# Optimization experiments

Measured on AMD Instinct MI355X. Metric: run time of the kernel, lower is better.

## Reference

```python
import jax, jax.numpy as jnp
import numpy as np

# dims
P = 512          # perception_vector_size
A_DIM = 64       # action_vector_size
D_MODEL = 256
D_STATE = 16
D_CONV = 4
D_INNER = 2 * D_MODEL      # expand=2 -> 512
DT_RANK = D_MODEL // 16    # ceil(256/16) = 16
BATCH = 8192


def setup_inputs() -> dict:
    key = jax.random.key(0)
    ks = jax.random.split(key, 12)
    s = lambda k, shp, sc=0.02: (jax.random.normal(k, shp, jnp.float32) * sc)
    return {
        "perception": jax.random.normal(ks[0], (BATCH, P), jnp.float32),
        # Brain linears
        "W_in": s(ks[1], (D_MODEL, P)), "b_in": jnp.zeros((D_MODEL,), jnp.float32),
        "mu_w": s(ks[2], (A_DIM, D_MODEL)), "mu_b": jnp.zeros((A_DIM,), jnp.float32),
        "ls_w": s(ks[3], (A_DIM, D_MODEL)), "ls_b": jnp.zeros((A_DIM,), jnp.float32),
        # Mamba params (mamba_ssm Mamba(d_model=256, d_state=16, d_conv=4, expand=2))
        "in_proj_w": s(ks[4], (2 * D_INNER, D_MODEL)),            # no bias
        "conv_w": s(ks[5], (D_INNER, D_CONV), 0.1),               # depthwise causal conv
        "conv_b": jnp.zeros((D_INNER,), jnp.float32),
        "x_proj_w": s(ks[6], (DT_RANK + 2 * D_STATE, D_INNER)),   # no bias
        "dt_proj_w": s(ks[7], (D_INNER, DT_RANK), 0.1),
        "dt_proj_b": s(ks[8], (D_INNER,), 0.1),
        # S4D real init: A_log[d, n] = log(n+1)
        "A_log": jnp.log(jnp.broadcast_to(jnp.arange(1, D_STATE + 1, dtype=jnp.float32), (D_INNER, D_STATE))),
        "Dskip": jnp.ones((D_INNER,), jnp.float32),
        "out_proj_w": s(ks[9], (D_MODEL, D_INNER)),               # no bias
    }


def _mamba(x, in_proj_w, conv_w, conv_b, x_proj_w, dt_proj_w, dt_proj_b, A_log, Dskip):
    # x: [B, L, d_model]
    Bsz, L, _ = x.shape
    xz = x @ in_proj_w.T                       # [B, L, 2*D_INNER]
    u, z = jnp.split(xz, 2, axis=-1)           # each [B, L, D_INNER]
    # causal depthwise conv1d (padding d_conv-1 on the left), then SiLU
    u_pad = jnp.pad(u, ((0, 0), (D_CONV - 1, 0), (0, 0)))
    idx = jnp.arange(L)[:, None] + jnp.arange(D_CONV)[None, :]   # [L, K]
    windows = u_pad[:, idx, :]                 # [B, L, K, D_INNER]
    u = jnp.einsum('blkc,ck->blc', windows, conv_w) + conv_b
    u = jax.nn.silu(u)
    # input-dependent SSM params
    x_dbl = u @ x_proj_w.T                     # [B, L, dt_rank + 2*d_state]
    dt, Bm, Cm = jnp.split(x_dbl, [DT_RANK, DT_RANK + D_STATE], axis=-1)
    delta = jax.nn.softplus(dt @ dt_proj_w.T + dt_proj_b)  # [B, L, D_INNER]
    A = -jnp.exp(A_log)                        # [D_INNER, D_STATE]

    def step(h, inp):
        u_t, dl, b_t, c_t = inp                # [B,D],[B,D],[B,N],[B,N]
        dA = jnp.exp(dl[..., None] * A)        # [B, D, N]
        h = dA * h + dl[..., None] * b_t[:, None, :] * u_t[..., None]
        y = jnp.einsum('bdn,bn->bd', h, c_t)
        return h, y

    h0 = jnp.zeros((Bsz, D_INNER, D_STATE), u.dtype)
    xs = (u.transpose(1, 0, 2), delta.transpose(1, 0, 2),
          Bm.transpose(1, 0, 2), Cm.transpose(1, 0, 2))
    _, ys = jax.lax.scan(step, h0, xs)         # ys: [L, B, D_INNER]
    y = ys.transpose(1, 0, 2) + Dskip * u      # skip connection D*u
    return y * jax.nn.silu(z)


def reference(perception, W_in, b_in, mu_w, mu_b, ls_w, ls_b,
              in_proj_w, conv_w, conv_b, x_proj_w, dt_proj_w, dt_proj_b,
              A_log, Dskip, out_proj_w):
    x = (perception @ W_in.T + b_in)[:, None, :]     # [B, 1, d_model]
    y = _mamba(x, in_proj_w, conv_w, conv_b, x_proj_w,
               dt_proj_w, dt_proj_b, A_log, Dskip)   # [B, 1, D_INNER]
    h = (y @ out_proj_w.T)[:, 0, :]                  # [B, d_model]
    mu = jnp.tanh(h @ mu_w.T + mu_b)
    log_std = jnp.clip(h @ ls_w.T + ls_b, -5.0, 2.0)
    return mu, log_std
```

## Files before the change

### kernel.cpp

```cpp
#include <hip/hip_runtime.h>
#include <hip/hip_fp16.h>
#include <cmath>

#define BATCH 8192

typedef short bf16x8 __attribute__((ext_vector_type(8)));
typedef float f32x4 __attribute__((ext_vector_type(4)));
typedef float f32x16 __attribute__((ext_vector_type(16)));

__device__ __forceinline__ void split2(float x, unsigned short& h, unsigned short& l){
    unsigned u = __float_as_uint(x);
    unsigned hr = u + 0x7fffu + ((u >> 16) & 1u);
    unsigned short hs = (unsigned short)(hr >> 16);
    float hf = __uint_as_float(((unsigned)hs) << 16);
    float d = x - hf;
    unsigned v = __float_as_uint(d);
    unsigned short ls = (unsigned short)((v + 0x7fffu + ((v >> 16) & 1u)) >> 16);
    h = hs; l = ls;
}
__device__ __forceinline__ float fsig(float x){ return 1.f / (1.f + __expf(-x)); }
__device__ __forceinline__ float ftanh(float x){
    x = fminf(fmaxf(x, -10.f), 10.f);
    const float e = __expf(2.f*x);
    return (e - 1.f) / (e + 1.f);
}


__global__ __launch_bounds__(256) void prep_all(
    const float* __restrict__ percep,
    const float* __restrict__ in_proj, const float* __restrict__ W_in,
    const float* __restrict__ b_in,
    const float* __restrict__ mu_w, const float* __restrict__ ls_w,
    const float* __restrict__ conv_w, const float* __restrict__ conv_b,
    const float* __restrict__ out_proj, const float* __restrict__ x_proj,
    unsigned short* __restrict__ W1h, unsigned short* __restrict__ W1l,
    unsigned short* __restrict__ Wth, unsigned short* __restrict__ Wtl,
    unsigned short* __restrict__ Xph, unsigned short* __restrict__ Xpl,
    unsigned short* __restrict__ Ph, unsigned short* __restrict__ Pl,
    float* __restrict__ b1)
{
    __shared__ float As[16][33];
    __shared__ float Ws[16][36];
    __shared__ unsigned short Lh[4096];
    __shared__ unsigned short Ll[4096];

    const int bx = blockIdx.x, by = blockIdx.y;
    const int tid = threadIdx.x;

    if (bx >= 38){
        const int s = (bx-38)*16 + by;
        const int band = s >> 4, ks = s & 15;
        const size_t tbase = (size_t)s*4096;
#pragma unroll
        for (int g=0; g<2; ++g){
            const int u = g*256 + tid;
            const int row = u >> 2, piece = u & 3;
            const float* src = percep + (size_t)(band*128 + row)*512 + ks*32 + piece*8;
            const float4 v0 = *reinterpret_cast<const float4*>(src);
            const float4 v1 = *reinterpret_cast<const float4*>(src+4);
            unsigned short h[8], l[8];
            split2(v0.x,h[0],l[0]); split2(v0.y,h[1],l[1]);
            split2(v0.z,h[2],l[2]); split2(v0.w,h[3],l[3]);
            split2(v1.x,h[4],l[4]); split2(v1.y,h[5],l[5]);
            split2(v1.z,h[6],l[6]); split2(v1.w,h[7],l[7]);
            uint4 H, L;
            H.x=(unsigned)h[0]|((unsigned)h[1]<<16); H.y=(unsigned)h[2]|((unsigned)h[3]<<16);
            H.z=(unsigned)h[4]|((unsigned)h[5]<<16); H.w=(unsigned)h[6]|((unsigned)h[7]<<16);
            L.x=(unsigned)l[0]|((unsigned)l[1]<<16); L.y=(unsigned)l[2]|((unsigned)l[3]<<16);
            L.z=(unsigned)l[4]|((unsigned)l[5]<<16); L.w=(unsigned)l[6]|((unsigned)l[7]<<16);
            const int off = piece*1024 + row*8;
            *reinterpret_cast<uint4*>(&Lh[off]) = H;
            *reinterpret_cast<uint4*>(&Ll[off]) = L;
        }
        __syncthreads();
#pragma unroll
        for (int g=0; g<2; ++g){
            const int f = g*256 + tid;
            *reinterpret_cast<uint4*>(&Ph[tbase + f*8]) = *reinterpret_cast<const uint4*>(&Lh[f*8]);
            *reinterpret_cast<uint4*>(&Pl[tbase + f*8]) = *reinterpret_cast<const uint4*>(&Ll[f*8]);
        }
        return;
    }
    if (bx == 36){
        const int lane = tid & 63, w = tid >> 6;
        const float4 bv = *reinterpret_cast<const float4*>(&b_in[lane*4]);
        const int nbase = by*64 + w*16;
#pragma unroll 4
        for (int i=0;i<16;i++){
            const int n = nbase + i;
            const float4 av = *reinterpret_cast<const float4*>(&in_proj[(size_t)n*256 + lane*4]);
            float p = av.x*bv.x + av.y*bv.y + av.z*bv.z + av.w*bv.w;
#pragma unroll
            for (int off=32; off; off>>=1) p += __shfl_xor(p, off, 64);
            if (lane == 0)
                b1[n] = (n < 512) ? fmaf(p, conv_w[n*4+3], conv_b[n]) : p;
        }
        return;
    }
    if (bx == 37){
        const int c0 = by*32;
#pragma unroll
        for (int p=0;p<8;p++){
            const int idx = p*256 + tid;
            const int rrow = idx >> 5;
            const int c = c0 + (idx & 31);
            const float v = (rrow < 48) ? x_proj[(size_t)rrow*512 + c] : 0.f;
            unsigned short h,l; split2(v,h,l);
            const int ks = c >> 5, r = (c >> 3) & 3, pos = c & 7;
            const size_t off = (size_t)ks*2048 + (r*64 + rrow)*8 + pos;
            Xph[off]=h; Xpl[off]=l;
        }
        return;
    }
    const float* A; unsigned short *Oh, *Ol; int m0; bool wt;
    const float* B;
    if (bx < 32){ A = in_proj + (size_t)bx*32*256; B = W_in; Oh=W1h; Ol=W1l; m0=bx*32; wt=false; }
    else {
        const int t = bx - 32;
        A = (t < 2) ? (mu_w + (size_t)t*32*256) : (ls_w + (size_t)(t-2)*32*256);
        B = out_proj; Oh=Wth; Ol=Wtl; m0=t*32; wt=true;
    }
    const int n0 = by*32;

    const int tm = tid >> 3, tn = tid & 7;
    float acc[4] = {0.f,0.f,0.f,0.f};

    for (int k0=0;k0<256;k0+=16){
        {
            const int row = tid >> 3, kf = (tid & 7)*2;
            const float2 v = *reinterpret_cast<const float2*>(A + (size_t)row*256 + k0 + kf);
            As[kf][row] = v.x; As[kf+1][row] = v.y;
        }
        {
            const int kk = tid >> 4, c = (tid & 15)*2;
            const float2 v = *reinterpret_cast<const float2*>(B + (size_t)(k0+kk)*512 + n0 + c);
            Ws[kk][c] = v.x; Ws[kk][c+1] = v.y;
        }
        __syncthreads();
#pragma unroll
        for (int k=0;k<16;k++){
            const float a = As[k][tm];
            const float4 bv = *reinterpret_cast<const float4*>(&Ws[k][tn*4]);
            acc[0] = fmaf(a, bv.x, acc[0]);
            acc[1] = fmaf(a, bv.y, acc[1]);
            acc[2] = fmaf(a, bv.z, acc[2]);
            acc[3] = fmaf(a, bv.w, acc[3]);
        }
        __syncthreads();
    }
    {
        const int gm = m0 + tm;
        const float s = (!wt && gm < 512) ? conv_w[gm*4+3] : 1.f;
        const int n = n0 + tn*4;
        unsigned short h[4], l[4];
#pragma unroll
        for (int j=0;j<4;j++) split2(acc[j]*s, h[j], l[j]);
        const int ks = n >> 5, r = (n >> 3) & 3, pos = n & 7;
        size_t off;
        if (wt) off = (size_t)ks*4096 + (r*128 + gm)*8 + pos;
        else    off = (size_t)((gm>>7)*16 + ks)*4096 + (r*128 + (gm&127))*8 + pos;
        *reinterpret_cast<ushort4*>(&Oh[off]) = make_ushort4(h[0],h[1],h[2],h[3]);
        *reinterpret_cast<ushort4*>(&Ol[off]) = make_ushort4(l[0],l[1],l[2],l[3]);
    }
}

__global__ __launch_bounds__(256,8) void mgemm6c(
    const unsigned short* __restrict__ AhT, const unsigned short* __restrict__ AlT,
    const unsigned short* __restrict__ BhT, const unsigned short* __restrict__ BlT,
    const float* __restrict__ bias,
    float* __restrict__ O0, __half* __restrict__ O1)
{
    constexpr int NK = 16;

    const int tid = threadIdx.x;
    const int mb = blockIdx.x, nb = blockIdx.y;
    const int m0 = mb * 32, n0 = nb * 128;
    const int lane = tid & 63, wid = tid >> 6;
    const int half = lane >> 5, l32 = lane & 31;
    const int wn = wid * 32;

    f32x16 acc;
#pragma unroll
    for (int r=0;r<16;r++) acc[r] = 0.f;

    const int gm = m0 + l32;
    const size_t Atile0 = (size_t)((gm>>7)*16)*4096;
    const int Ain = (gm & 127)*8;
    const unsigned short* Bh0 = BhT + (size_t)nb*NK*4096;
    const unsigned short* Bl0 = BlT + (size_t)nb*NK*4096;

#pragma unroll
    for (int k=0; k<NK; ++k){
        const size_t at = Atile0 + (size_t)k*4096 + Ain;
        bf16x8 ah[2], al[2], bh[2], bl[2];
#pragma unroll
        for (int j=0;j<2;j++){
            const int r = j*2 + half;
            ah[j] = *reinterpret_cast<const bf16x8*>(&AhT[at + r*1024]);
            al[j] = *reinterpret_cast<const bf16x8*>(&AlT[at + r*1024]);
            const size_t off = (size_t)k*4096 + (r*128 + wn + l32)*8;
            bh[j] = *reinterpret_cast<const bf16x8*>(&Bh0[off]);
            bl[j] = *reinterpret_cast<const bf16x8*>(&Bl0[off]);
        }
#pragma unroll
        for (int j=0;j<2;j++){
            acc = __builtin_amdgcn_mfma_f32_32x32x16_bf16(ah[j], bh[j], acc, 0,0,0);
            acc = __builtin_amdgcn_mfma_f32_32x32x16_bf16(al[j], bh[j], acc, 0,0,0);
            acc = __builtin_amdgcn_mfma_f32_32x32x16_bf16(ah[j], bl[j], acc, 0,0,0);
        }
    }

#pragma unroll
    for (int r=0; r<16; ++r){
        const int row = m0 + (r&3) + 8*(r>>2) + 4*half;
        const int col = n0 + wn + l32;
        float v = acc[r] + bias[col];
        if (col < 512) O0[(size_t)row*512 + col] = v * fsig(v);
        else           O1[(size_t)row*512 + (col-512)] = __float2half(v);
    }
}

__global__ __launch_bounds__(256,2) void tail_fused3(
    const float* __restrict__ Uf, const __half* __restrict__ Zh,
    const unsigned short* __restrict__ XphT, const unsigned short* __restrict__ XplT,
    const unsigned short* __restrict__ WthT, const unsigned short* __restrict__ WtlT,
    const float* __restrict__ dtw, const float* __restrict__ dtb,
    const float* __restrict__ dskip,
    const float* __restrict__ mu_b, const float* __restrict__ ls_b,
    float* __restrict__ mu_o, float* __restrict__ ls_o)
{
    constexpr int TM = 16;
    constexpr int ROWB = 136;
    __shared__ unsigned short sYh[2][16*ROWB];
    __shared__ unsigned short sYl[2][16*ROWB];
    __shared__ float sxd[TM][49];
    __shared__ float sBC[TM];

    const int tid = threadIdx.x;
    const int m0 = blockIdx.x * TM;
    const int lane = tid & 63, wid = tid >> 6;
    const int quad = lane >> 4, l16 = lane & 15;
    const int q = wid;

    float2 uvp[4][4]; __half2 zvp[4][4];
#pragma unroll
    for (int c=0;c<4;++c){
        const int d0 = c*128 + 2*lane;
#pragma unroll
        for (int rr=0; rr<4; ++rr){
            const size_t off = (size_t)(m0 + q*4 + rr)*512 + d0;
            uvp[c][rr] = *reinterpret_cast<const float2*>(&Uf[off]);
            zvp[c][rr] = *reinterpret_cast<const __half2*>(&Zh[off]);
        }
    }
    float2 dbp[4], dkp[4];
#pragma unroll
    for (int c=0;c<4;++c){
        const int d0 = c*128 + 2*lane;
        dbp[c] = *reinterpret_cast<const float2*>(&dtb[d0]);
        dkp[c] = *reinterpret_cast<const float2*>(&dskip[d0]);
    }

    f32x4 acc = (f32x4){0.f,0.f,0.f,0.f};
    const float* arow = Uf + (size_t)(m0 + l16)*512 + quad*8;
    const int bxp = (quad*64 + wid*16 + l16)*8;
#pragma unroll
    for (int k=0; k<16; ++k){
        const float4 a0 = *reinterpret_cast<const float4*>(arow + k*32);
        const float4 a1 = *reinterpret_cast<const float4*>(arow + k*32 + 4);
        const bf16x8 bh = *reinterpret_cast<const bf16x8*>(&XphT[(size_t)k*2048 + bxp]);
        const bf16x8 bl = *reinterpret_cast<const bf16x8*>(&XplT[(size_t)k*2048 + bxp]);
        bf16x8 ah, al;
        {
            const float a[8] = {a0.x,a0.y,a0.z,a0.w,a1.x,a1.y,a1.z,a1.w};
            unsigned short h[8], l[8];
#pragma unroll
            for (int j=0;j<8;j++) split2(a[j], h[j], l[j]);
#pragma unroll
            for (int j=0;j<8;j++){ ah[j] = (short)h[j]; al[j] = (short)l[j]; }
        }
        acc = __builtin_amdgcn_mfma_f32_16x16x32_bf16(ah, bh, acc, 0,0,0);
        acc = __builtin_amdgcn_mfma_f32_16x16x32_bf16(al, bh, acc, 0,0,0);
        acc = __builtin_amdgcn_mfma_f32_16x16x32_bf16(ah, bl, acc, 0,0,0);
    }

    {
        const int colp = wid*16 + l16;
        if (colp < 48){
#pragma unroll
            for (int r=0;r<4;++r) sxd[quad*4 + r][colp] = acc[r];
        }
    }
    __syncthreads();
    if (tid < TM){
        float bc = 0.f;
#pragma unroll
        for (int n=0;n<16;n++) bc = fmaf(sxd[tid][16+n], sxd[tid][32+n], bc);
        sBC[tid] = bc;
    }
    __syncthreads();

    f32x4 oacc[2];
    oacc[0] = (f32x4){0.f,0.f,0.f,0.f};
    oacc[1] = (f32x4){0.f,0.f,0.f,0.f};

    const unsigned ybase = (unsigned)(lane >> 2)*68 + (unsigned)(lane & 3);

#pragma unroll
    for (int c=0; c<4; ++c){
        const int d0 = c*128 + 2*lane, d1 = d0 + 1;
        float w0[16], w1[16];
#pragma unroll
        for (int j=0;j<4;j++){
            const float4 a = *reinterpret_cast<const float4*>(&dtw[d0*16 + j*4]);
            w0[j*4]=a.x; w0[j*4+1]=a.y; w0[j*4+2]=a.z; w0[j*4+3]=a.w;
            const float4 b = *reinterpret_cast<const float4*>(&dtw[d1*16 + j*4]);
            w1[j*4]=b.x; w1[j*4+1]=b.y; w1[j*4+2]=b.z; w1[j*4+3]=b.w;
        }
        const float db0 = dbp[c].x, db1 = dbp[c].y;
        const float dk0 = dkp[c].x, dk1 = dkp[c].y;

        unsigned short* yh = sYh[c&1];
        unsigned short* yl = sYl[c&1];
#pragma unroll
        for (int rr=0; rr<4; ++rr){
            const int r = q*4 + rr;
            float xr[16];
#pragma unroll
            for (int j=0;j<16;j++) xr[j] = sxd[r][j];
            const float bc = sBC[r];
            float t0 = db0, t1 = db1;
#pragma unroll
            for (int j=0;j<16;j++){ t0 = fmaf(xr[j], w0[j], t0); t1 = fmaf(xr[j], w1[j], t1); }
            const float dl0 = (t0 > 20.f) ? t0 : __logf(1.f + __expf(t0));
            const float dl1 = (t1 > 20.f) ? t1 : __logf(1.f + __expf(t1));
            const float2 uv = uvp[c][rr];
            const __half2 zv = zvp[c][rr];
            const float z0 = __low2float(zv), z1 = __high2float(zv);
            const float y0 = uv.x * fmaf(dl0, bc, dk0) * (z0 * fsig(z0));
            const float y1 = uv.y * fmaf(dl1, bc, dk1) * (z1 * fsig(z1));
            unsigned short h0,l0,h1,l1;
            split2(y0,h0,l0); split2(y1,h1,l1);
            reinterpret_cast<unsigned*>(yh)[ybase + r*4] = (unsigned)h0 | ((unsigned)h1<<16);
            reinterpret_cast<unsigned*>(yl)[ybase + r*4] = (unsigned)l0 | ((unsigned)l1<<16);
        }
        __syncthreads();

#pragma unroll
        for (int s=0; s<4; ++s){
            const int kt = c*4 + s;
            const int aoff = (4*s + quad)*ROWB + l16*8;
            const bf16x8 ya = *reinterpret_cast<const bf16x8*>(&yh[aoff]);
            const bf16x8 yl8 = *reinterpret_cast<const bf16x8*>(&yl[aoff]);
            bf16x8 bh2[2], bl2[2];
#pragma unroll
            for (int nt=0; nt<2; ++nt){
                const size_t boff = (size_t)kt*4096 + (quad*128 + wid*32 + nt*16 + l16)*8;
                bh2[nt] = *reinterpret_cast<const bf16x8*>(&WthT[boff]);
                bl2[nt] = *reinterpret_cast<const bf16x8*>(&WtlT[boff]);
            }
#pragma unroll
            for (int nt=0; nt<2; ++nt)
                oacc[nt] = __builtin_amdgcn_mfma_f32_16x16x32_bf16(ya, bh2[nt], oacc[nt], 0,0,0);
#pragma unroll
            for (int nt=0; nt<2; ++nt)
                oacc[nt] = __builtin_amdgcn_mfma_f32_16x16x32_bf16(yl8, bh2[nt], oacc[nt], 0,0,0);
#pragma unroll
            for (int nt=0; nt<2; ++nt)
                oacc[nt] = __builtin_amdgcn_mfma_f32_16x16x32_bf16(ya, bl2[nt], oacc[nt], 0,0,0);
        }
    }

#pragma unroll
    for (int nt=0; nt<2; ++nt)
#pragma unroll
    for (int r=0; r<4; ++r){
        const int row = m0 + quad*4 + r;
        const int col = wid*32 + nt*16 + l16;
        const float v = oacc[nt][r];
        if (col < 64) mu_o[(size_t)row*64 + col] = ftanh(v + mu_b[col]);
        else          ls_o[(size_t)row*64 + (col-64)] = fminf(fmaxf(v + ls_b[col-64], -5.f), 2.f);
    }
}

extern "C" void kernel_launch(void* const* d_in, const int* in_sizes, int n_in,
                              void* d_out, int out_size, void* d_ws, size_t ws_size,
                              hipStream_t stream) {
    (void)in_sizes; (void)n_in; (void)out_size; (void)ws_size;
    const float* percep  = (const float*)d_in[0];
    const float* W_in    = (const float*)d_in[1];
    const float* b_in    = (const float*)d_in[2];
    const float* mu_w    = (const float*)d_in[3];
    const float* mu_b    = (const float*)d_in[4];
    const float* ls_w    = (const float*)d_in[5];
    const float* ls_b    = (const float*)d_in[6];
    const float* in_proj = (const float*)d_in[7];
    const float* conv_w  = (const float*)d_in[8];
    const float* conv_b  = (const float*)d_in[9];
    const float* x_proj  = (const float*)d_in[10];
    const float* dt_w    = (const float*)d_in[11];
    const float* dt_b    = (const float*)d_in[12];
    const float* Dskip   = (const float*)d_in[14];
    const float* out_proj= (const float*)d_in[15];

    char* ws = (char*)d_ws;
    const size_t MB = 1u<<20;
    unsigned short* W1h = (unsigned short*)(ws);
    unsigned short* W1l = (unsigned short*)(ws + 1*MB);
    unsigned short* Wth = (unsigned short*)(ws + 2*MB);
    unsigned short* Wtl = (unsigned short*)(ws + 2*MB + 128*1024);
    unsigned short* Xph = (unsigned short*)(ws + 2*MB + 256*1024);
    unsigned short* Xpl = (unsigned short*)(ws + 2*MB + 320*1024);
    float*          b1  = (float*)         (ws + 2*MB + 384*1024);
    unsigned short* Ph  = (unsigned short*)(ws + 4*MB);
    unsigned short* Pl  = (unsigned short*)(ws + 12*MB);
    float*          Uf  = (float*)         (ws + 20*MB);
    __half*         Zh  = (__half*)        (ws + 36*MB);

    float* mu_o = (float*)d_out;
    float* ls_o = (float*)d_out + (size_t)BATCH*64;

    dim3 blk(256);
    prep_all<<<dim3(102,16), blk, 0, stream>>>(
        percep, in_proj, W_in, b_in, mu_w, ls_w, conv_w, conv_b, out_proj, x_proj,
        W1h, W1l, Wth, Wtl, Xph, Xpl, Ph, Pl, b1);
    mgemm6c<<<dim3(256,8), blk, 0, stream>>>(
        Ph, Pl, W1h, W1l, b1, Uf, Zh);
    tail_fused3<<<dim3(BATCH/16), blk, 0, stream>>>(
        Uf, Zh, Xph, Xpl, Wth, Wtl, dt_w, dt_b, Dskip, mu_b, ls_b, mu_o, ls_o);
}
```

Baseline: 174.5 us.

## Fuse main projection GEMM into tail kernel, keeping U and Z in shared memory

Removes the separate mgemm6c kernel and computes the 16-row slice of the big in_proj GEMM inside the tail kernel. The U (SiLU) and Z results go to padded LDS instead of round-tripping through global memory, which removes one launch and the Uf/Zh write and re-read traffic. In exchange each 16-row block re-reads the whole weight matrix (1024x512 hi/lo). It also uses thin 16-row MFMA tiles with 16 accumulators per wave, and the added LDS use may lower occupancy.

```diff
diff --git a/kernel.cpp b/kernel.cpp
--- a/kernel.cpp
+++ b/kernel.cpp
@@ -6,7 +6,6 @@
 
 typedef short bf16x8 __attribute__((ext_vector_type(8)));
 typedef float f32x4 __attribute__((ext_vector_type(4)));
-typedef float f32x16 __attribute__((ext_vector_type(16)));
 
 __device__ __forceinline__ void split2(float x, unsigned short& h, unsigned short& l){
     unsigned u = __float_as_uint(x);
@@ -164,64 +163,10 @@
     }
 }
 
-__global__ __launch_bounds__(256,8) void mgemm6c(
-    const unsigned short* __restrict__ AhT, const unsigned short* __restrict__ AlT,
-    const unsigned short* __restrict__ BhT, const unsigned short* __restrict__ BlT,
-    const float* __restrict__ bias,
-    float* __restrict__ O0, __half* __restrict__ O1)
-{
-    constexpr int NK = 16;
-
-    const int tid = threadIdx.x;
-    const int mb = blockIdx.x, nb = blockIdx.y;
-    const int m0 = mb * 32, n0 = nb * 128;
-    const int lane = tid & 63, wid = tid >> 6;
-    const int half = lane >> 5, l32 = lane & 31;
-    const int wn = wid * 32;
-
-    f32x16 acc;
-#pragma unroll
-    for (int r=0;r<16;r++) acc[r] = 0.f;
-
-    const int gm = m0 + l32;
-    const size_t Atile0 = (size_t)((gm>>7)*16)*4096;
-    const int Ain = (gm & 127)*8;
-    const unsigned short* Bh0 = BhT + (size_t)nb*NK*4096;
-    const unsigned short* Bl0 = BlT + (size_t)nb*NK*4096;
-
-#pragma unroll
-    for (int k=0; k<NK; ++k){
-        const size_t at = Atile0 + (size_t)k*4096 + Ain;
-        bf16x8 ah[2], al[2], bh[2], bl[2];
-#pragma unroll
-        for (int j=0;j<2;j++){
-            const int r = j*2 + half;
-            ah[j] = *reinterpret_cast<const bf16x8*>(&AhT[at + r*1024]);
-            al[j] = *reinterpret_cast<const bf16x8*>(&AlT[at + r*1024]);
-            const size_t off = (size_t)k*4096 + (r*128 + wn + l32)*8;
-            bh[j] = *reinterpret_cast<const bf16x8*>(&Bh0[off]);
-            bl[j] = *reinterpret_cast<const bf16x8*>(&Bl0[off]);
-        }
-#pragma unroll
-        for (int j=0;j<2;j++){
-            acc = __builtin_amdgcn_mfma_f32_32x32x16_bf16(ah[j], bh[j], acc, 0,0,0);
-            acc = __builtin_amdgcn_mfma_f32_32x32x16_bf16(al[j], bh[j], acc, 0,0,0);
-            acc = __builtin_amdgcn_mfma_f32_32x32x16_bf16(ah[j], bl[j], acc, 0,0,0);
-        }
-    }
-
-#pragma unroll
-    for (int r=0; r<16; ++r){
-        const int row = m0 + (r&3) + 8*(r>>2) + 4*half;
-        const int col = n0 + wn + l32;
-        float v = acc[r] + bias[col];
-        if (col < 512) O0[(size_t)row*512 + col] = v * fsig(v);
-        else           O1[(size_t)row*512 + (col-512)] = __float2half(v);
-    }
-}
-
-__global__ __launch_bounds__(256,2) void tail_fused3(
-    const float* __restrict__ Uf, const __half* __restrict__ Zh,
+__global__ __launch_bounds__(256,2) void mtail_fused(
+    const unsigned short* __restrict__ Ph, const unsigned short* __restrict__ Pl,
+    const unsigned short* __restrict__ W1h, const unsigned short* __restrict__ W1l,
+    const float* __restrict__ b1,
     const unsigned short* __restrict__ XphT, const unsigned short* __restrict__ XplT,
     const unsigned short* __restrict__ WthT, const unsigned short* __restrict__ WtlT,
     const float* __restrict__ dtw, const float* __restrict__ dtb,
@@ -231,6 +176,10 @@
 {
     constexpr int TM = 16;
     constexpr int ROWB = 136;
+    constexpr int UPAD = 516;
+    constexpr int ZPAD = 520;
+    __shared__ float sU[16*UPAD];
+    __shared__ __half sZ[16*ZPAD];
     __shared__ unsigned short sYh[2][16*ROWB];
     __shared__ unsigned short sYl[2][16*ROWB];
     __shared__ float sxd[TM][49];
@@ -242,15 +191,52 @@
     const int quad = lane >> 4, l16 = lane & 15;
     const int q = wid;
 
+    {
+        const int band = m0 >> 7, rowin = m0 & 127;
+        f32x4 vacc[16];
+#pragma unroll
+        for (int ct=0; ct<16; ++ct) vacc[ct] = (f32x4){0.f,0.f,0.f,0.f};
+
+        for (int ks=0; ks<16; ++ks){
+            const size_t at = (size_t)(band*16+ks)*4096 + (quad*128 + rowin + l16)*8;
+            const bf16x8 ah = *reinterpret_cast<const bf16x8*>(&Ph[at]);
+            const bf16x8 al = *reinterpret_cast<const bf16x8*>(&Pl[at]);
+#pragma unroll
+            for (int ct=0; ct<16; ++ct){
+                const int ncol = wid*256 + ct*16;
+                const int nb = ncol >> 7, nin = ncol & 127;
+                const size_t bt = (size_t)(nb*16+ks)*4096 + (quad*128 + nin + l16)*8;
+                const bf16x8 bh = *reinterpret_cast<const bf16x8*>(&W1h[bt]);
+                const bf16x8 bl = *reinterpret_cast<const bf16x8*>(&W1l[bt]);
+                vacc[ct] = __builtin_amdgcn_mfma_f32_16x16x32_bf16(ah, bh, vacc[ct], 0,0,0);
+                vacc[ct] = __builtin_amdgcn_mfma_f32_16x16x32_bf16(al, bh, vacc[ct], 0,0,0);
+                vacc[ct] = __builtin_amdgcn_mfma_f32_16x16x32_bf16(ah, bl, vacc[ct], 0,0,0);
+            }
+        }
+#pragma unroll
+        for (int ct=0; ct<16; ++ct){
+            const int n = wid*256 + ct*16 + l16;
+            const float bb = b1[n];
+#pragma unroll
+            for (int r=0;r<4;++r){
+                const int row = quad*4 + r;
+                const float v = vacc[ct][r] + bb;
+                if (n < 512) sU[row*UPAD + n] = v * fsig(v);
+                else         sZ[row*ZPAD + (n-512)] = __float2half(v);
+            }
+        }
+    }
+    __syncthreads();
+
     float2 uvp[4][4]; __half2 zvp[4][4];
 #pragma unroll
     for (int c=0;c<4;++c){
         const int d0 = c*128 + 2*lane;
 #pragma unroll
         for (int rr=0; rr<4; ++rr){
-            const size_t off = (size_t)(m0 + q*4 + rr)*512 + d0;
-            uvp[c][rr] = *reinterpret_cast<const float2*>(&Uf[off]);
-            zvp[c][rr] = *reinterpret_cast<const __half2*>(&Zh[off]);
+            const int r = q*4 + rr;
+            uvp[c][rr] = make_float2(sU[r*UPAD + d0], sU[r*UPAD + d0 + 1]);
+            zvp[c][rr] = *reinterpret_cast<const __half2*>(&sZ[r*ZPAD + d0]);
         }
     }
     float2 dbp[4], dkp[4];
@@ -262,7 +248,7 @@
     }
 
     f32x4 acc = (f32x4){0.f,0.f,0.f,0.f};
-    const float* arow = Uf + (size_t)(m0 + l16)*512 + quad*8;
+    const float* arow = &sU[l16*UPAD + quad*8];
     const int bxp = (quad*64 + wid*16 + l16)*8;
 #pragma unroll
     for (int k=0; k<16; ++k){
@@ -350,7 +336,7 @@
         for (int s=0; s<4; ++s){
             const int kt = c*4 + s;
             const int aoff = (4*s + quad)*ROWB + l16*8;
-            const bf16x8 ya = *reinterpret_cast<const bf16x8*>(&yh[aoff]);
+            const bf16x8 ya  = *reinterpret_cast<const bf16x8*>(&yh[aoff]);
             const bf16x8 yl8 = *reinterpret_cast<const bf16x8*>(&yl[aoff]);
             bf16x8 bh2[2], bl2[2];
 #pragma unroll
@@ -414,8 +400,6 @@
     float*          b1  = (float*)         (ws + 2*MB + 384*1024);
     unsigned short* Ph  = (unsigned short*)(ws + 4*MB);
     unsigned short* Pl  = (unsigned short*)(ws + 12*MB);
-    float*          Uf  = (float*)         (ws + 20*MB);
-    __half*         Zh  = (__half*)        (ws + 36*MB);
 
     float* mu_o = (float*)d_out;
     float* ls_o = (float*)d_out + (size_t)BATCH*64;
@@ -424,8 +408,7 @@
     prep_all<<<dim3(102,16), blk, 0, stream>>>(
         percep, in_proj, W_in, b_in, mu_w, ls_w, conv_w, conv_b, out_proj, x_proj,
         W1h, W1l, Wth, Wtl, Xph, Xpl, Ph, Pl, b1);
-    mgemm6c<<<dim3(256,8), blk, 0, stream>>>(
-        Ph, Pl, W1h, W1l, b1, Uf, Zh);
-    tail_fused3<<<dim3(BATCH/16), blk, 0, stream>>>(
-        Uf, Zh, Xph, Xpl, Wth, Wtl, dt_w, dt_b, Dskip, mu_b, ls_b, mu_o, ls_o);
+    mtail_fused<<<dim3(BATCH/16), blk, 0, stream>>>(
+        Ph, Pl, W1h, W1l, b1, Xph, Xpl, Wth, Wtl,
+        dt_w, dt_b, Dskip, mu_b, ls_b, mu_o, ls_o);
 }
```

After: 194.9 us. +11.7%, slower.
